# Performance work log

Measured on AMD Instinct MI355X. Metric: run time of the kernel, lower is better.

Reference implementation:

```python
import jax, jax.numpy as jnp
import numpy as np

B, T, D, KDIM = 256, 512, 256, 256

def setup_inputs() -> dict:
    key = jax.random.key(0)
    k1, k2, k3 = jax.random.split(key, 3)
    inputs = jax.random.normal(k1, (B, T, D), dtype=jnp.float32)
    # glorot-style scaling for stability of the recurrence
    U = jax.random.normal(k2, (D, KDIM), dtype=jnp.float32) * (1.0 / np.sqrt(D))
    W = jax.random.normal(k3, (KDIM, KDIM), dtype=jnp.float32) * (1.0 / np.sqrt(KDIM))
    b = jnp.zeros((KDIM,), dtype=jnp.float32)
    return {"inputs": inputs, "U": U, "W": W, "b": b}

def reference(inputs, U, W, b):
    # vanilla RNN: h_t = tanh(x_t U + h_{t-1} W + b); returns final hidden state
    xU = jnp.einsum('btd,dk->btk', inputs, U) + b  # precompute input projection [B,T,K]

    def step(h, xu_t):
        h = jnp.tanh(xu_t + h @ W)
        return h, None

    h0 = jnp.zeros((inputs.shape[0], W.shape[0]), dtype=inputs.dtype)
    h_final, _ = jax.lax.scan(step, h0, jnp.swapaxes(xU, 0, 1))  # scan over time
    # original keras code keeps a singleton time axis on the state: [B,1,K]
    return h_final[:, None, :]
```

## Files before the change

kernel.cpp:

```cpp
#include <hip/hip_runtime.h>
#include <hip/hip_bf16.h>


typedef _Float16 half8_t __attribute__((ext_vector_type(8)));
typedef _Float16 half2_t __attribute__((ext_vector_type(2)));
typedef float    float4_t __attribute__((ext_vector_type(4)));

#define MFMA16(a, b, c) __builtin_amdgcn_mfma_f32_16x16x32_f16((a), (b), (c), 0, 0, 0)

__device__ __forceinline__ half2_t pk_h2(float a, float b) {
    auto r = __builtin_amdgcn_cvt_pkrtz(a, b);
    return __builtin_bit_cast(half2_t, r);
}

__device__ __forceinline__ float fast_tanh(float x) {
    float e = __builtin_amdgcn_exp2f(2.8853900817779268f * x);
    return 1.0f - 2.0f * __builtin_amdgcn_rcpf(e + 1.0f);
}

__device__ __forceinline__ void lds_barrier() {
    __builtin_amdgcn_sched_barrier(0);
    asm volatile("s_waitcnt lgkmcnt(0)" ::: "memory");
    __builtin_amdgcn_s_barrier();
    __builtin_amdgcn_sched_barrier(0);
}

__global__ void transpose_u(const float* __restrict__ U, _Float16* __restrict__ Ut) {
    int id = blockIdx.x * 256 + threadIdx.x;
    int d = id >> 8, n = id & 255;
    Ut[n * 264 + d] = (_Float16)U[id];
}

__global__ __launch_bounds__(256, 2) void xu_gemm(
    const float* __restrict__ x,
    const _Float16* __restrict__ Ut,
    const float* __restrict__ bias,
    half2_t* __restrict__ xu)
{
    __shared__ char lds[61440];
    const int tid = threadIdx.x;
    const int lane = tid & 63, w = tid >> 6, l15 = lane & 15, q = lane >> 4;
    const int bx = blockIdx.x;
    const size_t m0 = (size_t)bx * 128;

    float4 ar[4];
    uint4  br[4];

    auto loadA = [&](int it) {
#pragma unroll
        for (int i = 0; i < 4; ++i) {
            int u = tid + 256 * i, row = u >> 3, seg = u & 7;
            ar[i] = *(const float4*)(x + (m0 + row) * 256 + it * 32 + seg * 4);
        }
    };
    auto loadB = [&](int it) {
#pragma unroll
        for (int i = 0; i < 4; ++i) {
            int u = tid + 256 * i, p = u >> 2, seg = u & 3;
            int c = 32 * (p >> 5) + 2 * (p & 15) + ((p >> 4) & 1);
            br[i] = *(const uint4*)((const char*)Ut + c * 528 + it * 64 + seg * 16);
        }
    };
    auto writeAB = [&](int s) {
        char* As = lds + s * 10240;
        char* Bs = lds + 20480 + s * 20480;
#pragma unroll
        for (int i = 0; i < 4; ++i) {
            int u = tid + 256 * i, row = u >> 3, seg = u & 7;
            half2_t p0 = pk_h2(ar[i].x, ar[i].y);
            half2_t p1 = pk_h2(ar[i].z, ar[i].w);
            uint2 v;
            v.x = __builtin_bit_cast(unsigned, p0);
            v.y = __builtin_bit_cast(unsigned, p1);
            *(uint2*)(As + row * 80 + seg * 8) = v;
        }
#pragma unroll
        for (int i = 0; i < 4; ++i) {
            int u = tid + 256 * i, p = u >> 2, seg = u & 3;
            *(uint4*)(Bs + p * 80 + seg * 16) = br[i];
        }
    };

    float4_t acc[32];
#pragma unroll
    for (int i = 0; i < 32; ++i) { acc[i][0] = 0.f; acc[i][1] = 0.f; acc[i][2] = 0.f; acc[i][3] = 0.f; }

    loadA(0); loadB(0); writeAB(0);
    __syncthreads();

    for (int it = 0; it < 8; ++it) {
        if (it < 7) { loadA(it + 1); loadB(it + 1); }
        const char* As = lds + (it & 1) * 10240;
        const char* Bs = lds + 20480 + (it & 1) * 20480;
        half8_t af[2];
#pragma unroll
        for (int ms = 0; ms < 2; ++ms)
            af[ms] = *(const half8_t*)(As + (32 * w + 16 * ms + l15) * 80 + q * 16);
#pragma unroll
        for (int ns = 0; ns < 16; ++ns) {
            half8_t bf = *(const half8_t*)(Bs + (16 * ns + l15) * 80 + q * 16);
            acc[ns * 2 + 0] = MFMA16(af[0], bf, acc[ns * 2 + 0]);
            acc[ns * 2 + 1] = MFMA16(af[1], bf, acc[ns * 2 + 1]);
        }
        if (it < 7) writeAB((it + 1) & 1);
        __syncthreads();
    }

#pragma unroll
    for (int ms = 0; ms < 2; ++ms)
#pragma unroll
        for (int j = 0; j < 8; ++j) {
            const int c = 32 * j + 2 * l15;
            const float2 bb = *(const float2*)(bias + c);
#pragma unroll
            for (int i = 0; i < 4; ++i) {
                float v0 = acc[(2 * j) * 2 + ms][i] + bb.x;
                float v1 = acc[(2 * j + 1) * 2 + ms][i] + bb.y;
                half2_t p = pk_h2(v0, v1);
                int m_g = bx * 128 + 32 * w + 16 * ms + q * 4 + i;
                xu[(size_t)m_g * 128 + (c >> 1)] = p;
            }
        }
}

__global__ __launch_bounds__(512, 2) void rnn_scan(
    const half2_t* __restrict__ xu,
    const float* __restrict__ W,
    float* __restrict__ out)
{
    __shared__ char lds[16896];
    const int tid = threadIdx.x;
    const int lane = tid & 63, w = tid >> 6, l15 = lane & 15, q = lane >> 4;
    const int blk = blockIdx.x;
    const int c0 = 32 * w + 2 * l15;

    half8_t wf[2][8];
#pragma unroll
    for (int tt = 0; tt < 2; ++tt)
#pragma unroll
        for (int c = 0; c < 8; ++c) {
            half8_t f;
#pragma unroll
            for (int j = 0; j < 8; ++j) {
                int k = 32 * c + q * 8 + j;
                f[j] = (_Float16)W[k * 256 + c0 + tt];
            }
            wf[tt][c] = f;
        }

    for (int i = tid; i < 16896 / 4; i += 512) ((int*)lds)[i] = 0;

    const int rowg0 = 16 * blk + q * 4;
    const int colh = c0 >> 1;

    unsigned xoff[4];
#pragma unroll
    for (int i = 0; i < 4; ++i)
        xoff[i] = (unsigned)(rowg0 + i) * 512u * 128u + (unsigned)colh;

    half2_t xr[4][4];
#pragma unroll
    for (int p = 0; p < 4; ++p)
#pragma unroll
        for (int i = 0; i < 4; ++i)
            xr[p][i] = xu[xoff[i] + (unsigned)p * 128u];
#pragma unroll
    for (int i = 0; i < 4; ++i) xoff[i] += 4u * 128u;

    char* const L = (char*)lds;
    const int afb = l15 * 528 + q * 16;
    const int hwb = (q * 4) * 528 + c0 * 2;

    __syncthreads();

#define SCAN_STEP(P_, PAR, DOPF, LAST)                                          \
    {                                                                           \
        const char* hcur = L + ((PAR) ? 8448 : 0);                              \
        half8_t af[8];                                                          \
        _Pragma("unroll")                                                       \
        for (int c8 = 0; c8 < 8; ++c8)                                          \
            af[c8] = *(const half8_t*)(hcur + afb + c8 * 64);                   \
        float4_t a0a, a1a, a0b, a1b;                                            \
        _Pragma("unroll")                                                       \
        for (int i = 0; i < 4; ++i) {                                           \
            a0a[i] = (float)xr[P_][i][0];                                       \
            a1a[i] = (float)xr[P_][i][1];                                       \
            a0b[i] = 0.f; a1b[i] = 0.f;                                         \
        }                                                                       \
        if (DOPF) {                                                             \
            _Pragma("unroll")                                                   \
            for (int i = 0; i < 4; ++i) {                                       \
                xr[P_][i] = xu[xoff[i]];                                        \
                xoff[i] += 128u;                                                \
            }                                                                   \
        }                                                                       \
        _Pragma("unroll")                                                       \
        for (int c = 0; c < 4; ++c) {                                           \
            a0a = MFMA16(af[2 * c],     wf[0][2 * c],     a0a);                 \
            a1a = MFMA16(af[2 * c],     wf[1][2 * c],     a1a);                 \
            a0b = MFMA16(af[2 * c + 1], wf[0][2 * c + 1], a0b);                 \
            a1b = MFMA16(af[2 * c + 1], wf[1][2 * c + 1], a1b);                 \
        }                                                                       \
        if (LAST) {                                                             \
            _Pragma("unroll")                                                   \
            for (int i = 0; i < 4; ++i) {                                       \
                float2 st;                                                      \
                st.x = fast_tanh(a0a[i] + a0b[i]);                              \
                st.y = fast_tanh(a1a[i] + a1b[i]);                              \
                *(float2*)(&out[(rowg0 + i) * 256 + c0]) = st;                  \
            }                                                                   \
        } else {                                                                \
            char* hnext = L + ((PAR) ? 0 : 8448);                               \
            _Pragma("unroll")                                                   \
            for (int i = 0; i < 4; ++i) {                                       \
                float v0 = fast_tanh(a0a[i] + a0b[i]);                          \
                float v1 = fast_tanh(a1a[i] + a1b[i]);                          \
                *(half2_t*)(hnext + hwb + i * 528) = pk_h2(v0, v1);             \
            }                                                                   \
            lds_barrier();                                                      \
        }                                                                       \
    }

    for (int t4 = 0; t4 < 508; t4 += 4) {
        SCAN_STEP(0, 0, 1, 0)
        SCAN_STEP(1, 1, 1, 0)
        SCAN_STEP(2, 0, 1, 0)
        SCAN_STEP(3, 1, 1, 0)
    }
    SCAN_STEP(0, 0, 0, 0)
    SCAN_STEP(1, 1, 0, 0)
    SCAN_STEP(2, 0, 0, 0)
    SCAN_STEP(3, 1, 0, 1)
#undef SCAN_STEP
}

extern "C" void kernel_launch(void* const* d_in, const int* in_sizes, int n_in,
                              void* d_out, int out_size, void* d_ws, size_t ws_size,
                              hipStream_t stream) {
    const float* x = (const float*)d_in[0];
    const float* U = (const float*)d_in[1];
    const float* W = (const float*)d_in[2];
    const float* b = (const float*)d_in[3];
    float* out = (float*)d_out;

    char* ws = (char*)d_ws;
    _Float16* Ut = (_Float16*)ws;
    half2_t*  xu = (half2_t*)(ws + 262144);

    transpose_u<<<256, 256, 0, stream>>>(U, Ut);
    xu_gemm<<<1024, 256, 0, stream>>>(x, Ut, b, xu);
    rnn_scan<<<16, 512, 0, stream>>>(xu, W, out);
}
```

Before: 519.9 us.

## Replace per-step workgroup barrier with per-wave LDS flag spin-waits in RNN scan

The scan kernel drops the s_barrier after every timestep. Instead, each wave publishes a step counter in a small LDS flag array and spins on the other waves' flags before reading the shared hidden state. The goal is to cut barrier stall time and let waves run ahead loosely instead of in lockstep. In exchange it adds polling LDS reads and relies on hand-written waitcnt ordering to keep the double-buffered state correct.

```diff
diff --git a/kernel.cpp b/kernel.cpp
--- a/kernel.cpp
+++ b/kernel.cpp
@@ -16,13 +16,6 @@
 __device__ __forceinline__ float fast_tanh(float x) {
     float e = __builtin_amdgcn_exp2f(2.8853900817779268f * x);
     return 1.0f - 2.0f * __builtin_amdgcn_rcpf(e + 1.0f);
-}
-
-__device__ __forceinline__ void lds_barrier() {
-    __builtin_amdgcn_sched_barrier(0);
-    asm volatile("s_waitcnt lgkmcnt(0)" ::: "memory");
-    __builtin_amdgcn_s_barrier();
-    __builtin_amdgcn_sched_barrier(0);
 }
 
 __global__ void transpose_u(const float* __restrict__ U, _Float16* __restrict__ Ut) {
@@ -128,7 +121,7 @@
     const float* __restrict__ W,
     float* __restrict__ out)
 {
-    __shared__ char lds[16896];
+    __shared__ char lds[16928];
     const int tid = threadIdx.x;
     const int lane = tid & 63, w = tid >> 6, l15 = lane & 15, q = lane >> 4;
     const int blk = blockIdx.x;
@@ -149,6 +142,7 @@
         }
 
     for (int i = tid; i < 16896 / 4; i += 512) ((int*)lds)[i] = 0;
+    if (tid < 8) *(int*)(lds + 16896 + tid * 4) = 0;
 
     const int rowg0 = 16 * blk + q * 4;
     const int colh = c0 >> 1;
@@ -165,16 +159,27 @@
         for (int i = 0; i < 4; ++i)
             xr[p][i] = xu[xoff[i] + (unsigned)p * 128u];
 #pragma unroll
-    for (int i = 0; i < 4; ++i) xoff[i] += 4u * 128u;
+    for (int i = 0; i < 4; ++i) xoff[i] += 512u;
 
     char* const L = (char*)lds;
     const int afb = l15 * 528 + q * 16;
     const int hwb = (q * 4) * 528 + c0 * 2;
+    const int fla = 16896 + (lane & 7) * 4;
+    const int flw = 16896 + w * 4;
+    const int notown = ((lane & 7) != w) ? 1 : 0;
 
     __syncthreads();
 
-#define SCAN_STEP(P_, PAR, DOPF, LAST)                                          \
+    int fpre = 0;
+
+#define READ_FLAG()                                                             \
+    asm volatile("ds_read_b32 %0, %1\n\ts_waitcnt lgkmcnt(0)"                   \
+                 : "=v"(fpre) : "v"(fla) : "memory")
+
+#define SCAN_STEP(P_, PAR, DOPF, LAST, T_)                                      \
     {                                                                           \
+        while (__ballot(notown && (fpre < (T_)))) { READ_FLAG(); }              \
+        asm volatile("" ::: "memory");   \
         const char* hcur = L + ((PAR) ? 8448 : 0);                              \
         half8_t af[8];                                                          \
         _Pragma("unroll")                                                       \
@@ -211,27 +216,36 @@
             }                                                                   \
         } else {                                                                \
             char* hnext = L + ((PAR) ? 0 : 8448);                               \
+                \
+                    \
+            asm volatile("ds_read_b32 %0, %1" : "=v"(fpre) : "v"(fla));         \
             _Pragma("unroll")                                                   \
             for (int i = 0; i < 4; ++i) {                                       \
                 float v0 = fast_tanh(a0a[i] + a0b[i]);                          \
                 float v1 = fast_tanh(a1a[i] + a1b[i]);                          \
                 *(half2_t*)(hnext + hwb + i * 528) = pk_h2(v0, v1);             \
             }                                                                   \
-            lds_barrier();                                                      \
+            asm volatile("s_waitcnt lgkmcnt(0)" ::: "memory");                  \
+            if (lane == 0) {                                                    \
+                int nv_ = (T_) + 1;                                             \
+                asm volatile("ds_write_b32 %0, %1"                              \
+                             :: "v"(flw), "v"(nv_) : "memory");                 \
+            }                                                                   \
         }                                                                       \
     }
 
     for (int t4 = 0; t4 < 508; t4 += 4) {
-        SCAN_STEP(0, 0, 1, 0)
-        SCAN_STEP(1, 1, 1, 0)
-        SCAN_STEP(2, 0, 1, 0)
-        SCAN_STEP(3, 1, 1, 0)
+        SCAN_STEP(0, 0, 1, 0, t4)
+        SCAN_STEP(1, 1, 1, 0, t4 + 1)
+        SCAN_STEP(2, 0, 1, 0, t4 + 2)
+        SCAN_STEP(3, 1, 1, 0, t4 + 3)
     }
-    SCAN_STEP(0, 0, 0, 0)
-    SCAN_STEP(1, 1, 0, 0)
-    SCAN_STEP(2, 0, 0, 0)
-    SCAN_STEP(3, 1, 0, 1)
+    SCAN_STEP(0, 0, 0, 0, 508)
+    SCAN_STEP(1, 1, 0, 0, 509)
+    SCAN_STEP(2, 0, 0, 0, 510)
+    SCAN_STEP(3, 1, 0, 1, 511)
 #undef SCAN_STEP
+#undef READ_FLAG
 }
 
 extern "C" void kernel_launch(void* const* d_in, const int* in_sizes, int n_in,
```

Result: slower. 542.5 us (+4.3%).
